# Kernel optimization log

Measured on AMD Instinct MI355X. Metric: run time of the kernel, lower is better.

Reference implementation:

```python
import jax, jax.numpy as jnp
import numpy as np

B, N, D = 1, 4096, 320
HEADS, DIM_HEAD = 8, 40
PHASE, Hm, Wm = 3, 64, 64  # guidance mask spatial dims; Hm*Wm == N


def setup_inputs() -> dict:
    key = jax.random.key(0)
    ks = jax.random.split(key, 7)
    s = 0.02
    x = jax.random.normal(ks[0], (B, N, D), jnp.float32)
    guidance_mask = jax.random.bernoulli(ks[1], 0.25, (B, PHASE, Hm, Wm)).astype(jnp.float32)
    Wq = jax.random.normal(ks[2], (D, HEADS * DIM_HEAD), jnp.float32) * s
    Wk = jax.random.normal(ks[3], (D, HEADS * DIM_HEAD), jnp.float32) * s
    Wv = jax.random.normal(ks[4], (D, HEADS * DIM_HEAD), jnp.float32) * s
    Wo = jax.random.normal(ks[5], (HEADS * DIM_HEAD, D), jnp.float32) * s
    bo = jnp.zeros((D,), jnp.float32)
    return {"x": x, "guidance_mask": guidance_mask, "Wq": Wq, "Wk": Wk,
            "Wv": Wv, "Wo": Wo, "bo": bo}


def reference(x, guidance_mask, Wq, Wk, Wv, Wo, bo):
    b, n, _ = x.shape
    h, dh = HEADS, DIM_HEAD
    scale = dh ** (-0.5)

    def split_heads(t):
        # b n (h d) -> (b h) n d
        return t.reshape(b, n, h, dh).transpose(0, 2, 1, 3).reshape(b * h, n, dh)

    q = split_heads(x @ Wq)
    k = split_heads(x @ Wk)
    v = split_heads(x @ Wv)

    sim = jnp.einsum('bid,bjd->bij', q, k) * scale  # (b*h, n, n)

    _, p, Hh, Ww = guidance_mask.shape
    HW = Hh * Ww  # == n
    g = guidance_mask.reshape(b, p, HW)
    # sum over phases of outer products, clamped at 1 (binary block mask)
    mask_sim = jnp.minimum(jnp.einsum('bpi,bpj->bij', g, g), 1.0)  # (b, HW, HW)
    mask_sim = jnp.repeat(mask_sim, h, axis=0)  # (b*h, HW, HW), heads within each b

    neg = -jnp.finfo(sim.dtype).max
    # original: sim[:, :, :HW][mask_sim == 0] = -max ; here n == HW so full matrix
    sim = jnp.where(mask_sim == 0, neg, sim)

    attn = jax.nn.softmax(sim, axis=-1)
    out = jnp.einsum('bij,bjd->bid', attn, v)  # (b*h, n, dh)
    out = out.reshape(b, h, n, dh).transpose(0, 2, 1, 3).reshape(b, n, h * dh)
    return out @ Wo + bo
```

## Files before the change

kernel.cpp:

```cpp
#include <hip/hip_runtime.h>
#include <hip/hip_bf16.h>
#include <stdint.h>

#define NT 4096
#define DM 320
#define NH 8
#define DH 40
#define KS 4
#define QSCALE 0.22811013f
#define PSTR 68
#define KFJB 640

typedef float f32x4 __attribute__((ext_vector_type(4)));
typedef __bf16 bf16x8 __attribute__((ext_vector_type(8)));

__device__ __forceinline__ unsigned short f2b(float f) {
  unsigned u = __builtin_bit_cast(unsigned, f);
  u += 0x7FFFu + ((u >> 16) & 1u);
  return (unsigned short)(u >> 16);
}

__device__ __forceinline__ bf16x8 ld_bf8(const unsigned short* p) {
  uint4 v = *(const uint4*)p;
  return __builtin_bit_cast(bf16x8, v);
}

__device__ __forceinline__ f32x4 mfma16(bf16x8 a, bf16x8 b, f32x4 c) {
  return __builtin_amdgcn_mfma_f32_16x16x32_bf16(a, b, c, 0, 0, 0);
}

__device__ __forceinline__ float fexp2(float x) {
#if __has_builtin(__builtin_amdgcn_exp2f)
  return __builtin_amdgcn_exp2f(x);
#else
  float r; asm("v_exp_f32 %0, %1" : "=v"(r) : "v"(x)); return r;
#endif
}

__device__ __forceinline__ uint2 pack4(float a, float b, float c, float d) {
  uint2 pk;
  pk.x = (unsigned)f2b(a) | ((unsigned)f2b(b) << 16);
  pk.y = (unsigned)f2b(c) | ((unsigned)f2b(d) << 16);
  return pk;
}

__device__ __forceinline__ size_t fmi(int tile, int nk, int k, int o) {
  return ((size_t)tile * nk + (k >> 5)) * 512 + (size_t)((k >> 3) & 3) * 128 +
         (size_t)(o & 15) * 8 + (k & 7);
}

__global__ __launch_bounds__(256) void prep_kernel(
    const float* __restrict__ x, const float* __restrict__ g,
    const float* __restrict__ Wq, const float* __restrict__ Wk,
    const float* __restrict__ Wv, const float* __restrict__ Wo,
    unsigned short* __restrict__ xbf, unsigned char* __restrict__ sgp,
    unsigned short* __restrict__ Wtf, int* __restrict__ perm,
    int* __restrict__ invp, int* __restrict__ nqp) {
  const int b = blockIdx.x, t = threadIdx.x;
  if (b == 100) {
    __shared__ int cnt[256];
    unsigned char mys[16];
    int c1 = 0;
#pragma unroll
    for (int i = 0; i < 16; ++i) {
      int tok = t * 16 + i;
      unsigned s = 0;
      if (g[tok] != 0.f)          s |= 1u;
      if (g[NT + tok] != 0.f)     s |= 2u;
      if (g[2 * NT + tok] != 0.f) s |= 4u;
      mys[i] = (unsigned char)s;
      c1 += (s != 0u);
    }
    cnt[t] = c1;
    __syncthreads();
    for (int off = 1; off < 256; off <<= 1) {
      int v = (t >= off) ? cnt[t - off] : 0;
      __syncthreads();
      cnt[t] += v;
      __syncthreads();
    }
    const int nq = cnt[255];
    int p1 = cnt[t] - c1;
    int p0 = nq + (t * 16 - p1);
#pragma unroll
    for (int i = 0; i < 16; ++i) {
      int tok = t * 16 + i;
      if (mys[i] != 0) { perm[p1] = tok; invp[tok] = p1; sgp[p1] = mys[i]; p1++; }
      else             { perm[p0] = tok; invp[tok] = p0; sgp[p0] = 0;      p0++; }
    }
    if (t == 0) nqp[0] = nq;
    return;
  }
  if (b > 100) {
    int base = (b - 101) * 2560;
#pragma unroll
    for (int j = 0; j < 10; ++j) {
      int i = (base + j * 256 + t) * 4;
      int m = i / DM, k = i % DM;
      float4 v = *(const float4*)(x + i);
      ushort4 u;
      u.x = f2b(v.x); u.y = f2b(v.y); u.z = f2b(v.z); u.w = f2b(v.w);
      *(ushort4*)(xbf + fmi(m >> 4, 10, k, m)) = u;
    }
    return;
  }
  __shared__ __align__(16) unsigned short lt[64 * 72];
  int kx = b % 5, cy = b / 5;
  int cm = cy % 5;
  const float* src;
  int rowbase;
  if (cy < 5)       { src = Wq; rowbase = cm * 64; }
  else if (cy < 10) { src = Wk; rowbase = 320 + cm * 64; }
  else if (cy < 15) { src = Wv; rowbase = 640 + cm * 64; }
  else              { src = Wo; rowbase = 960 + cm * 64; }
  const int c0 = cm * 64;
  const int k0 = kx * 64;
#pragma unroll
  for (int i = 0; i < 4; ++i) {
    int kr = (t >> 4) + i * 16, cc = (t & 15) * 4;
    float4 w4 = *(const float4*)&src[(size_t)(k0 + kr) * DM + c0 + cc];
    lt[(cc + 0) * 72 + kr] = f2b(w4.x);
    lt[(cc + 1) * 72 + kr] = f2b(w4.y);
    lt[(cc + 2) * 72 + kr] = f2b(w4.z);
    lt[(cc + 3) * 72 + kr] = f2b(w4.w);
  }
  __syncthreads();
#pragma unroll
  for (int i = 0; i < 2; ++i) {
    int idx = t + i * 256, cl = idx >> 3, ch = idx & 7;
    int c = rowbase + cl, k = k0 + ch * 8;
    *(uint4*)&Wtf[fmi(c >> 4, 10, k, c)] = *(const uint4*)&lt[cl * 72 + ch * 8];
  }
}

__global__ __launch_bounds__(256, 4) void qkv_gemm(
    const unsigned short* __restrict__ xbf, const unsigned short* __restrict__ Wtf,
    const int* __restrict__ invp,
    unsigned short* __restrict__ Qb, unsigned short* __restrict__ Kf,
    unsigned short* __restrict__ Vf) {
  const int t = threadIdx.x;
  const int w = t >> 6, lane = t & 63, quad = lane >> 4, ln = lane & 15;
  const int m0 = blockIdx.x * 64;
  const int cy = blockIdx.y;
  const int a = cy / 5;
  const int cc0 = (cy % 5) * 64;
  const int mt = (m0 >> 4) + w;
  const int ct0 = a * 20 + (cc0 >> 4);

  f32x4 acc[4] = {{0,0,0,0},{0,0,0,0},{0,0,0,0},{0,0,0,0}};
  for (int kc = 0; kc < 10; ++kc) {
    bf16x8 xf = ld_bf8(xbf + ((size_t)(mt * 10 + kc)) * 512 + lane * 8);
#pragma unroll
    for (int nt = 0; nt < 4; ++nt) {
      bf16x8 wf = ld_bf8(Wtf + ((size_t)((ct0 + nt) * 10 + kc)) * 512 + lane * 8);
      if (a < 2) acc[nt] = mfma16(wf, xf, acc[nt]);
      else       acc[nt] = mfma16(xf, wf, acc[nt]);
    }
  }
  if (a == 0) {
    const int bp = invp[m0 + w * 16 + ln];
#pragma unroll
    for (int nt = 0; nt < 4; ++nt) {
      int c = cc0 + nt * 16 + quad * 4;
      int h = c / DH, d = c % DH;
      uint2 pk = pack4(acc[nt][0] * QSCALE, acc[nt][1] * QSCALE,
                       acc[nt][2] * QSCALE, acc[nt][3] * QSCALE);
      *(uint2*)&Qb[((size_t)h * NT + bp) * 64 + d] = pk;
    }
  } else if (a == 1) {
    const int bp = invp[m0 + w * 16 + ln];
#pragma unroll
    for (int nt = 0; nt < 4; ++nt) {
      int c = cc0 + nt * 16 + quad * 4;
      int h = c / DH, d = c % DH;
      uint2 pk = pack4(acc[nt][0], acc[nt][1], acc[nt][2], acc[nt][3]);
      size_t base = ((size_t)h * 256 + (bp >> 4)) * KFJB;
      size_t idx = (d < 32)
          ? base + (size_t)(d >> 3) * 128 + (size_t)(bp & 15) * 8 + (d & 7)
          : base + 512 + (size_t)(bp & 15) * 8 + (d - 32);
      *(uint2*)&Kf[idx] = pk;
    }
  } else {
    const int mb = m0 + w * 16 + quad * 4;
    int bpr[4];
#pragma unroll
    for (int r = 0; r < 4; ++r) bpr[r] = invp[mb + r];
#pragma unroll
    for (int nt = 0; nt < 4; ++nt) {
      int c = cc0 + nt * 16 + ln;
      int h = c / DH, d = c % DH;
#pragma unroll
      for (int r = 0; r < 4; ++r) {
        int bp = bpr[r];
        size_t idx = ((((((size_t)(h * 64 + (bp >> 6)) * 3 + (d >> 4)) * 2 +
                         ((bp >> 5) & 1)) * 4 + ((bp >> 3) & 3)) * 16 + (d & 15))) * 8 +
                     (bp & 7);
        Vf[idx] = f2b(acc[nt][r]);
      }
    }
  }
}

__global__ __launch_bounds__(256, 4) void attn_kernel(
    const unsigned short* __restrict__ Qb, const unsigned short* __restrict__ Kf,
    const unsigned short* __restrict__ Vf, const unsigned char* __restrict__ sgp,
    const int* __restrict__ perm, const int* __restrict__ nqp,
    unsigned short* __restrict__ Opf, float* __restrict__ Lpart,
    unsigned short* __restrict__ Ubf) {
  __shared__ __align__(16) unsigned short pt[4][32 * PSTR];
  __shared__ float vs[4][48];
  const int t = threadIdx.x;
  const int w = t >> 6, lane = t & 63, quad = lane >> 4, ln = lane & 15;
  const int h = blockIdx.y, sp = blockIdx.z;
  const int nq = nqp[0];
  const int nkt = (nq + 63) >> 6;
  const int nq_pad = (nq + 127) & ~127;

  const unsigned short* Vfh = Vf + (size_t)h * 196608;
  const uint4 z4 = {0, 0, 0, 0};
  const uint4 ones4 = {0x3F803F80u, 0x3F803F80u, 0x3F803F80u, 0x3F803F80u};
  const bf16x8 onesb = __builtin_bit_cast(bf16x8, ones4);

  if (blockIdx.x == 32) {
    if (sp != 0) return;
    f32x4 o[3] = {{0,0,0,0},{0,0,0,0},{0,0,0,0}};
    for (int jt = w; jt < 64; jt += 4) {
#pragma unroll
      for (int ot = 0; ot < 3; ++ot) {
        uint4 v0 = *(const uint4*)(Vfh + ((size_t)((jt * 3 + ot) * 2 + 0)) * 512 +
                                   lane * 8);
        uint4 v1 = *(const uint4*)(Vfh + ((size_t)((jt * 3 + ot) * 2 + 1)) * 512 +
                                   lane * 8);
        o[ot] = mfma16(__builtin_bit_cast(bf16x8, v0), onesb, o[ot]);
        o[ot] = mfma16(__builtin_bit_cast(bf16x8, v1), onesb, o[ot]);
      }
    }
    if (ln == 0) {
#pragma unroll
      for (int ot = 0; ot < 3; ++ot)
#pragma unroll
        for (int r = 0; r < 4; ++r) vs[w][ot * 16 + quad * 4 + r] = o[ot][r];
    }
    __syncthreads();
    if (t < DH) {
      float s = vs[0][t] + vs[1][t] + vs[2][t] + vs[3][t];
      Ubf[h * DH + t] = f2b(s * (1.0f / (float)NT));
    }
    return;
  }

  const int qt = (blockIdx.x + 8 * sp) & 31;
  if (qt * 128 >= nq_pad) return;
  const int qrow = qt * 128 + w * 32;

  const unsigned short* Kfh = Kf + (size_t)h * 256 * KFJB;
  unsigned short* ptw = pt[w];
  const bool vone = (ln == 8);

  bf16x8 qa[2][2];
  unsigned sqx4[2];
  int morig[2];
  f32x4 o[3][2] = {{{0,0,0,0},{0,0,0,0}},{{0,0,0,0},{0,0,0,0}},{{0,0,0,0},{0,0,0,0}}};

#pragma unroll
  for (int tq = 0; tq < 2; ++tq) {
    int bp = qrow + tq * 16 + ln;
    morig[tq] = perm[bp];
    const unsigned short* Qp = Qb + ((size_t)h * NT + bp) * 64;
    qa[tq][0] = ld_bf8(Qp + quad * 8);
    uint4 q1 = z4;
    if (quad == 0) q1 = *(const uint4*)(Qp + 32);
    qa[tq][1] = __builtin_bit_cast(bf16x8, q1);
    sqx4[tq] = (unsigned)sgp[bp] * 0x01010101u;
  }

  for (int jt = sp; jt < nkt; jt += KS) {
    uint4 kfr0[4], kfr1[4];
#pragma unroll
    for (int nt = 0; nt < 4; ++nt) {
      const unsigned short* kb = Kfh + (size_t)(jt * 4 + nt) * KFJB;
      kfr0[nt] = *(const uint4*)(kb + lane * 8);
      kfr1[nt] = z4;
      if (lane < 16) kfr1[nt] = *(const uint4*)(kb + 512 + lane * 8);
    }
#pragma unroll
    for (int nt = 0; nt < 4; ++nt) {
      bf16x8 ka0 = __builtin_bit_cast(bf16x8, kfr0[nt]);
      bf16x8 ka1 = __builtin_bit_cast(bf16x8, kfr1[nt]);
      unsigned spj = *(const unsigned*)(sgp + jt * 64 + nt * 16 + quad * 4);
#pragma unroll
      for (int tq = 0; tq < 2; ++tq) {
        f32x4 acc = {0.f, 0.f, 0.f, 0.f};
        acc = mfma16(ka0, qa[tq][0], acc);
        acc = mfma16(ka1, qa[tq][1], acc);
        unsigned m4 = spj & sqx4[tq];
        unsigned u[4];
#pragma unroll
        for (int r = 0; r < 4; ++r) {
          unsigned mb = (m4 >> (8 * r)) & 255u;
          float am = mb ? acc[r] : -3.0e38f;
          u[r] = __builtin_bit_cast(unsigned, fexp2(am));
        }
        uint2 pk;
        pk.x = (u[0] >> 16) | (u[1] & 0xffff0000u);
        pk.y = (u[2] >> 16) | (u[3] & 0xffff0000u);
        *(uint2*)&ptw[(tq * 16 + ln) * PSTR + nt * 16 + quad * 4] = pk;
      }
    }
    uint4 vfr[6];
#pragma unroll
    for (int ot = 0; ot < 3; ++ot)
#pragma unroll
      for (int c = 0; c < 2; ++c)
        vfr[ot * 2 + c] =
            *(const uint4*)(Vfh + ((size_t)((jt * 3 + ot) * 2 + c)) * 512 + lane * 8);
    if (vone) { vfr[4] = ones4; vfr[5] = ones4; }

    bf16x8 pb[2][2];
    asm volatile("s_waitcnt lgkmcnt(0)" ::: "memory");
#pragma unroll
    for (int tq = 0; tq < 2; ++tq) {
      pb[tq][0] = ld_bf8(&ptw[(tq * 16 + ln) * PSTR + quad * 8]);
      pb[tq][1] = ld_bf8(&ptw[(tq * 16 + ln) * PSTR + 32 + quad * 8]);
    }
#pragma unroll
    for (int ot = 0; ot < 3; ++ot) {
      bf16x8 va0 = __builtin_bit_cast(bf16x8, vfr[ot * 2]);
      bf16x8 va1 = __builtin_bit_cast(bf16x8, vfr[ot * 2 + 1]);
#pragma unroll
      for (int tq = 0; tq < 2; ++tq) {
        o[ot][tq] = mfma16(va0, pb[tq][0], o[ot][tq]);
        o[ot][tq] = mfma16(va1, pb[tq][1], o[ot][tq]);
      }
    }
  }

#pragma unroll
  for (int tq = 0; tq < 2; ++tq) {
    int m = morig[tq];
#pragma unroll
    for (int ot = 0; ot < 3; ++ot) {
      int d0 = ot * 16 + quad * 4;
      if (d0 < DH) {
        int c = h * DH + d0;
        uint2 pk = pack4(o[ot][tq][0], o[ot][tq][1], o[ot][tq][2], o[ot][tq][3]);
        *(uint2*)&Opf[fmi(sp * 256 + (m >> 4), 10, c, m)] = pk;
      }
    }
    if (quad == 2)
      Lpart[sp * NT + m] = o[2][tq][0];
  }
}

__global__ __launch_bounds__(256, 4) void out_gemm(
    const unsigned short* __restrict__ Opf, const float* __restrict__ Lpart,
    const unsigned short* __restrict__ Wtf, const float* __restrict__ bo,
    const int* __restrict__ invp, const int* __restrict__ nqp,
    const unsigned short* __restrict__ Ubf, float* __restrict__ out) {
  const int t = threadIdx.x;
  const int w = t >> 6, lane = t & 63, quad = lane >> 4, ln = lane & 15;
  const int m0 = blockIdx.x * 64;
  const int cc0 = blockIdx.y * 64;
  const int mt = (m0 >> 4) + w;
  const int m = m0 + w * 16 + ln;
  const int ct0 = 60 + (cc0 >> 4);
  const bool uni = invp[m] >= nqp[0];
  float ls = 0.f;
#pragma unroll
  for (int sp = 0; sp < KS; ++sp) ls += Lpart[sp * NT + m];
  const float inv = 1.f / ls;

  f32x4 acc[4] = {{0,0,0,0},{0,0,0,0},{0,0,0,0},{0,0,0,0}};
  for (int kc = 0; kc < 10; ++kc) {
    uint4 uv = *(const uint4*)(Ubf + kc * 32 + quad * 8);
    float s8[8] = {0, 0, 0, 0, 0, 0, 0, 0};
#pragma unroll
    for (int sp = 0; sp < KS; ++sp) {
      uint4 v = *(const uint4*)(Opf + ((size_t)((sp * 256 + mt) * 10 + kc)) * 512 +
                                lane * 8);
      unsigned vv[4] = {v.x, v.y, v.z, v.w};
#pragma unroll
      for (int j = 0; j < 4; ++j) {
        s8[2 * j]     += __builtin_bit_cast(float, vv[j] << 16);
        s8[2 * j + 1] += __builtin_bit_cast(float, vv[j] & 0xffff0000u);
      }
    }
    uint4 av;
    av.x = (unsigned)f2b(s8[0] * inv) | ((unsigned)f2b(s8[1] * inv) << 16);
    av.y = (unsigned)f2b(s8[2] * inv) | ((unsigned)f2b(s8[3] * inv) << 16);
    av.z = (unsigned)f2b(s8[4] * inv) | ((unsigned)f2b(s8[5] * inv) << 16);
    av.w = (unsigned)f2b(s8[6] * inv) | ((unsigned)f2b(s8[7] * inv) << 16);
    if (uni) av = uv;
    bf16x8 af = __builtin_bit_cast(bf16x8, av);
#pragma unroll
    for (int nt = 0; nt < 4; ++nt) {
      bf16x8 wf = ld_bf8(Wtf + ((size_t)((ct0 + nt) * 10 + kc)) * 512 + lane * 8);
      acc[nt] = mfma16(wf, af, acc[nt]);
    }
  }
#pragma unroll
  for (int nt = 0; nt < 4; ++nt) {
    int c = cc0 + nt * 16 + quad * 4;
    float4 bv = *(const float4*)(bo + c);
    float4 ov;
    ov.x = acc[nt][0] + bv.x;
    ov.y = acc[nt][1] + bv.y;
    ov.z = acc[nt][2] + bv.z;
    ov.w = acc[nt][3] + bv.w;
    *(float4*)(out + (size_t)m * DM + c) = ov;
  }
}

extern "C" void kernel_launch(void* const* d_in, const int* in_sizes, int n_in,
                              void* d_out, int out_size, void* d_ws, size_t ws_size,
                              hipStream_t stream) {
  const float* x  = (const float*)d_in[0];
  const float* g  = (const float*)d_in[1];
  const float* Wq = (const float*)d_in[2];
  const float* Wk = (const float*)d_in[3];
  const float* Wv = (const float*)d_in[4];
  const float* Wo = (const float*)d_in[5];
  const float* bo = (const float*)d_in[6];
  float* out = (float*)d_out;

  char* ws = (char*)d_ws;
  const size_t SGP_OFF  = 0;
  const size_t NQ_OFF   = 4096;
  const size_t PERM_OFF = 8192;
  const size_t INV_OFF  = 24576;
  const size_t XBF_OFF  = 40960;
  const size_t WTF_OFF = XBF_OFF + (size_t)NT * DM * 2;
  const size_t QB_OFF  = WTF_OFF + (size_t)1280 * DM * 2;
  const size_t KF_OFF  = QB_OFF + (size_t)NH * NT * 64 * 2;
  const size_t VF_OFF  = KF_OFF + (size_t)NH * 256 * KFJB * 2;
  const size_t OPF_OFF = VF_OFF + (size_t)NH * 196608 * 2;
  const size_t LP_OFF  = OPF_OFF + (size_t)KS * 256 * 10 * 512 * 2;
  const size_t UBF_OFF = LP_OFF + (size_t)KS * NT * 4;
  unsigned char* sgp   = (unsigned char*)(ws + SGP_OFF);
  int* nqp             = (int*)(ws + NQ_OFF);
  int* perm            = (int*)(ws + PERM_OFF);
  int* invp            = (int*)(ws + INV_OFF);
  unsigned short* xbf  = (unsigned short*)(ws + XBF_OFF);
  unsigned short* Wtf  = (unsigned short*)(ws + WTF_OFF);
  unsigned short* Qb   = (unsigned short*)(ws + QB_OFF);
  unsigned short* Kf   = (unsigned short*)(ws + KF_OFF);
  unsigned short* Vf   = (unsigned short*)(ws + VF_OFF);
  unsigned short* Opf  = (unsigned short*)(ws + OPF_OFF);
  float* Lpart         = (float*)(ws + LP_OFF);
  unsigned short* Ubf  = (unsigned short*)(ws + UBF_OFF);

  prep_kernel<<<229, 256, 0, stream>>>(x, g, Wq, Wk, Wv, Wo, xbf, sgp, Wtf,
                                       perm, invp, nqp);
  qkv_gemm<<<dim3(64, 15), 256, 0, stream>>>(xbf, Wtf, invp, Qb, Kf, Vf);
  attn_kernel<<<dim3(33, NH, KS), 256, 0, stream>>>(Qb, Kf, Vf, sgp, perm, nqp,
                                                    Opf, Lpart, Ubf);
  out_gemm<<<dim3(64, 5), 256, 0, stream>>>(Opf, Lpart, Wtf, bo, invp, nqp,
                                            Ubf, out);
}
```

Before: 135.8 us.

## Move V retiling and split-K combine into separate coalesced kernels

The QKV GEMM now writes V in the same fragment layout as K, using uint2 stores instead of scattered 2-byte stores. A new retile kernel uses identity-matrix MFMAs to transpose V into the layout the attention kernel expects. The split-K partial combine and row un-permutation move out of the output GEMM into a dedicated combine kernel that writes a bf16 fragment buffer. Attention now writes outputs in permuted order. This trades extra launches and an extra round trip through global memory for coalesced writes and less redundant combine work across the output GEMM's column blocks.

```diff
diff --git a/kernel.cpp b/kernel.cpp
--- a/kernel.cpp
+++ b/kernel.cpp
@@ -42,6 +42,15 @@
   pk.x = (unsigned)f2b(a) | ((unsigned)f2b(b) << 16);
   pk.y = (unsigned)f2b(c) | ((unsigned)f2b(d) << 16);
   return pk;
+}
+
+__device__ __forceinline__ uint4 idfrag(int idx) {
+  uint4 r;
+  r.x = (idx == 0 ? 0x3F80u : 0u) | (idx == 1 ? 0x3F800000u : 0u);
+  r.y = (idx == 2 ? 0x3F80u : 0u) | (idx == 3 ? 0x3F800000u : 0u);
+  r.z = (idx == 4 ? 0x3F80u : 0u) | (idx == 5 ? 0x3F800000u : 0u);
+  r.w = (idx == 6 ? 0x3F80u : 0u) | (idx == 7 ? 0x3F800000u : 0u);
+  return r;
 }
 
 __device__ __forceinline__ size_t fmi(int tile, int nk, int k, int o) {
@@ -137,7 +146,7 @@
     const unsigned short* __restrict__ xbf, const unsigned short* __restrict__ Wtf,
     const int* __restrict__ invp,
     unsigned short* __restrict__ Qb, unsigned short* __restrict__ Kf,
-    unsigned short* __restrict__ Vf) {
+    unsigned short* __restrict__ Vk) {
   const int t = threadIdx.x;
   const int w = t >> 6, lane = t & 63, quad = lane >> 4, ln = lane & 15;
   const int m0 = blockIdx.x * 64;
@@ -153,12 +162,11 @@
 #pragma unroll
     for (int nt = 0; nt < 4; ++nt) {
       bf16x8 wf = ld_bf8(Wtf + ((size_t)((ct0 + nt) * 10 + kc)) * 512 + lane * 8);
-      if (a < 2) acc[nt] = mfma16(wf, xf, acc[nt]);
-      else       acc[nt] = mfma16(xf, wf, acc[nt]);
-    }
-  }
+      acc[nt] = mfma16(wf, xf, acc[nt]);
+    }
+  }
+  const int bp = invp[m0 + w * 16 + ln];
   if (a == 0) {
-    const int bp = invp[m0 + w * 16 + ln];
 #pragma unroll
     for (int nt = 0; nt < 4; ++nt) {
       int c = cc0 + nt * 16 + quad * 4;
@@ -167,8 +175,8 @@
                        acc[nt][2] * QSCALE, acc[nt][3] * QSCALE);
       *(uint2*)&Qb[((size_t)h * NT + bp) * 64 + d] = pk;
     }
-  } else if (a == 1) {
-    const int bp = invp[m0 + w * 16 + ln];
+  } else {
+    unsigned short* dst = (a == 1) ? Kf : Vk;
 #pragma unroll
     for (int nt = 0; nt < 4; ++nt) {
       int c = cc0 + nt * 16 + quad * 4;
@@ -178,25 +186,40 @@
       size_t idx = (d < 32)
           ? base + (size_t)(d >> 3) * 128 + (size_t)(bp & 15) * 8 + (d & 7)
           : base + 512 + (size_t)(bp & 15) * 8 + (d - 32);
-      *(uint2*)&Kf[idx] = pk;
-    }
-  } else {
-    const int mb = m0 + w * 16 + quad * 4;
-    int bpr[4];
-#pragma unroll
-    for (int r = 0; r < 4; ++r) bpr[r] = invp[mb + r];
-#pragma unroll
-    for (int nt = 0; nt < 4; ++nt) {
-      int c = cc0 + nt * 16 + ln;
-      int h = c / DH, d = c % DH;
-#pragma unroll
-      for (int r = 0; r < 4; ++r) {
-        int bp = bpr[r];
-        size_t idx = ((((((size_t)(h * 64 + (bp >> 6)) * 3 + (d >> 4)) * 2 +
-                         ((bp >> 5) & 1)) * 4 + ((bp >> 3) & 3)) * 16 + (d & 15))) * 8 +
-                     (bp & 7);
-        Vf[idx] = f2b(acc[nt][r]);
-      }
+      *(uint2*)&dst[idx] = pk;
+    }
+  }
+}
+
+__global__ __launch_bounds__(256) void retile_kernel(
+    const unsigned short* __restrict__ Vk, unsigned short* __restrict__ Vf) {
+  const int t = threadIdx.x;
+  const int w = t >> 6, lane = t & 63, ln = lane & 15, jg = lane >> 4;
+  const bf16x8 b1f = __builtin_bit_cast(bf16x8, idfrag(ln - jg * 8));
+  const bf16x8 b2f = __builtin_bit_cast(bf16x8, idfrag(ln + 16 - jg * 8));
+  const uint4 z4 = {0, 0, 0, 0};
+#pragma unroll
+  for (int i = 0; i < 4; ++i) {
+    const int task = (blockIdx.x * 4 + w) * 4 + i;
+    const int h = task >> 8, jb = task & 255;
+    const unsigned short* kb = Vk + ((size_t)h * 256 + jb) * KFJB;
+    uint4 f0 = *(const uint4*)(kb + lane * 8);
+    uint4 f1 = z4;
+    if (lane < 16) f1 = *(const uint4*)(kb + 512 + lane * 8);
+    f32x4 d1 = {0,0,0,0}, d2 = {0,0,0,0}, d3 = {0,0,0,0};
+    d1 = mfma16(__builtin_bit_cast(bf16x8, f0), b1f, d1);
+    d2 = mfma16(__builtin_bit_cast(bf16x8, f0), b2f, d2);
+    d3 = mfma16(__builtin_bit_cast(bf16x8, f1), b1f, d3);
+    const int bp = jb * 16 + jg * 4;
+#pragma unroll
+    for (int ot = 0; ot < 3; ++ot) {
+      int dd = ot * 16 + ln;
+      if (ot == 2 && ln >= 8) continue;
+      f32x4 dv = (ot == 0) ? d1 : (ot == 1) ? d2 : d3;
+      size_t idx = ((((((size_t)(h * 64 + (bp >> 6)) * 3 + (dd >> 4)) * 2 +
+                       ((bp >> 5) & 1)) * 4 + ((bp >> 3) & 3)) * 16 + (dd & 15))) * 8 +
+                   (bp & 7);
+      *(uint2*)&Vf[idx] = pack4(dv[0], dv[1], dv[2], dv[3]);
     }
   }
 }
@@ -204,7 +227,7 @@
 __global__ __launch_bounds__(256, 4) void attn_kernel(
     const unsigned short* __restrict__ Qb, const unsigned short* __restrict__ Kf,
     const unsigned short* __restrict__ Vf, const unsigned char* __restrict__ sgp,
-    const int* __restrict__ perm, const int* __restrict__ nqp,
+    const int* __restrict__ nqp,
     unsigned short* __restrict__ Opf, float* __restrict__ Lpart,
     unsigned short* __restrict__ Ubf) {
   __shared__ __align__(16) unsigned short pt[4][32 * PSTR];
@@ -259,13 +282,11 @@
 
   bf16x8 qa[2][2];
   unsigned sqx4[2];
-  int morig[2];
   f32x4 o[3][2] = {{{0,0,0,0},{0,0,0,0}},{{0,0,0,0},{0,0,0,0}},{{0,0,0,0},{0,0,0,0}}};
 
 #pragma unroll
   for (int tq = 0; tq < 2; ++tq) {
     int bp = qrow + tq * 16 + ln;
-    morig[tq] = perm[bp];
     const unsigned short* Qp = Qb + ((size_t)h * NT + bp) * 64;
     qa[tq][0] = ld_bf8(Qp + quad * 8);
     uint4 q1 = z4;
@@ -337,26 +358,64 @@
 
 #pragma unroll
   for (int tq = 0; tq < 2; ++tq) {
-    int m = morig[tq];
+    int bp = qrow + tq * 16 + ln;
 #pragma unroll
     for (int ot = 0; ot < 3; ++ot) {
       int d0 = ot * 16 + quad * 4;
       if (d0 < DH) {
         int c = h * DH + d0;
         uint2 pk = pack4(o[ot][tq][0], o[ot][tq][1], o[ot][tq][2], o[ot][tq][3]);
-        *(uint2*)&Opf[fmi(sp * 256 + (m >> 4), 10, c, m)] = pk;
+        *(uint2*)&Opf[fmi(sp * 256 + (bp >> 4), 10, c, bp)] = pk;
       }
     }
     if (quad == 2)
-      Lpart[sp * NT + m] = o[2][tq][0];
-  }
+      Lpart[sp * NT + bp] = o[2][tq][0];
+  }
+}
+
+__global__ __launch_bounds__(256, 4) void combine_kernel(
+    const unsigned short* __restrict__ Opf, const float* __restrict__ Lpart,
+    const int* __restrict__ perm, const int* __restrict__ nqp,
+    unsigned short* __restrict__ Abf) {
+  const int t = threadIdx.x;
+  const int w = t >> 6, lane = t & 63;
+  const int task = blockIdx.x * 4 + w;
+  const int tile = task / 10, kc = task % 10;
+  const int nq_pad = (nqp[0] + 127) & ~127;
+  if (tile * 16 >= nq_pad) return;
+  const int row = tile * 16 + (lane & 15);
+
+  float L = 0.f;
+#pragma unroll
+  for (int sp = 0; sp < KS; ++sp) L += Lpart[sp * NT + row];
+  const float inv = 1.f / L;
+
+  float s8[8] = {0, 0, 0, 0, 0, 0, 0, 0};
+#pragma unroll
+  for (int sp = 0; sp < KS; ++sp) {
+    uint4 v = *(const uint4*)(Opf + ((size_t)((sp * 256 + tile) * 10 + kc)) * 512 +
+                              lane * 8);
+    unsigned vv[4] = {v.x, v.y, v.z, v.w};
+#pragma unroll
+    for (int j = 0; j < 4; ++j) {
+      s8[2 * j]     += __builtin_bit_cast(float, vv[j] << 16);
+      s8[2 * j + 1] += __builtin_bit_cast(float, vv[j] & 0xffff0000u);
+    }
+  }
+  uint4 av;
+  av.x = (unsigned)f2b(s8[0] * inv) | ((unsigned)f2b(s8[1] * inv) << 16);
+  av.y = (unsigned)f2b(s8[2] * inv) | ((unsigned)f2b(s8[3] * inv) << 16);
+  av.z = (unsigned)f2b(s8[4] * inv) | ((unsigned)f2b(s8[5] * inv) << 16);
+  av.w = (unsigned)f2b(s8[6] * inv) | ((unsigned)f2b(s8[7] * inv) << 16);
+  const int m = perm[row];
+  *(uint4*)&Abf[fmi(m >> 4, 10, kc * 32 + (lane >> 4) * 8, m)] = av;
 }
 
 __global__ __launch_bounds__(256, 4) void out_gemm(
-    const unsigned short* __restrict__ Opf, const float* __restrict__ Lpart,
-    const unsigned short* __restrict__ Wtf, const float* __restrict__ bo,
-    const int* __restrict__ invp, const int* __restrict__ nqp,
-    const unsigned short* __restrict__ Ubf, float* __restrict__ out) {
+    const unsigned short* __restrict__ Abf, const unsigned short* __restrict__ Wtf,
+    const float* __restrict__ bo, const int* __restrict__ invp,
+    const int* __restrict__ nqp, const unsigned short* __restrict__ Ubf,
+    float* __restrict__ out) {
   const int t = threadIdx.x;
   const int w = t >> 6, lane = t & 63, quad = lane >> 4, ln = lane & 15;
   const int m0 = blockIdx.x * 64;
@@ -365,31 +424,11 @@
   const int m = m0 + w * 16 + ln;
   const int ct0 = 60 + (cc0 >> 4);
   const bool uni = invp[m] >= nqp[0];
-  float ls = 0.f;
-#pragma unroll
-  for (int sp = 0; sp < KS; ++sp) ls += Lpart[sp * NT + m];
-  const float inv = 1.f / ls;
 
   f32x4 acc[4] = {{0,0,0,0},{0,0,0,0},{0,0,0,0},{0,0,0,0}};
   for (int kc = 0; kc < 10; ++kc) {
     uint4 uv = *(const uint4*)(Ubf + kc * 32 + quad * 8);
-    float s8[8] = {0, 0, 0, 0, 0, 0, 0, 0};
-#pragma unroll
-    for (int sp = 0; sp < KS; ++sp) {
-      uint4 v = *(const uint4*)(Opf + ((size_t)((sp * 256 + mt) * 10 + kc)) * 512 +
-                                lane * 8);
-      unsigned vv[4] = {v.x, v.y, v.z, v.w};
-#pragma unroll
-      for (int j = 0; j < 4; ++j) {
-        s8[2 * j]     += __builtin_bit_cast(float, vv[j] << 16);
-        s8[2 * j + 1] += __builtin_bit_cast(float, vv[j] & 0xffff0000u);
-      }
-    }
-    uint4 av;
-    av.x = (unsigned)f2b(s8[0] * inv) | ((unsigned)f2b(s8[1] * inv) << 16);
-    av.y = (unsigned)f2b(s8[2] * inv) | ((unsigned)f2b(s8[3] * inv) << 16);
-    av.z = (unsigned)f2b(s8[4] * inv) | ((unsigned)f2b(s8[5] * inv) << 16);
-    av.w = (unsigned)f2b(s8[6] * inv) | ((unsigned)f2b(s8[7] * inv) << 16);
+    uint4 av = *(const uint4*)(Abf + ((size_t)(mt * 10 + kc)) * 512 + lane * 8);
     if (uni) av = uv;
     bf16x8 af = __builtin_bit_cast(bf16x8, av);
 #pragma unroll
@@ -432,10 +471,12 @@
   const size_t WTF_OFF = XBF_OFF + (size_t)NT * DM * 2;
   const size_t QB_OFF  = WTF_OFF + (size_t)1280 * DM * 2;
   const size_t KF_OFF  = QB_OFF + (size_t)NH * NT * 64 * 2;
-  const size_t VF_OFF  = KF_OFF + (size_t)NH * 256 * KFJB * 2;
+  const size_t VK_OFF  = KF_OFF + (size_t)NH * 256 * KFJB * 2;
+  const size_t VF_OFF  = VK_OFF + (size_t)NH * 256 * KFJB * 2;
   const size_t OPF_OFF = VF_OFF + (size_t)NH * 196608 * 2;
   const size_t LP_OFF  = OPF_OFF + (size_t)KS * 256 * 10 * 512 * 2;
   const size_t UBF_OFF = LP_OFF + (size_t)KS * NT * 4;
+  const size_t ABF_OFF = UBF_OFF + 4096;
   unsigned char* sgp   = (unsigned char*)(ws + SGP_OFF);
   int* nqp             = (int*)(ws + NQ_OFF);
   int* perm            = (int*)(ws + PERM_OFF);
@@ -444,16 +485,19 @@
   unsigned short* Wtf  = (unsigned short*)(ws + WTF_OFF);
   unsigned short* Qb   = (unsigned short*)(ws + QB_OFF);
   unsigned short* Kf   = (unsigned short*)(ws + KF_OFF);
+  unsigned short* Vk   = (unsigned short*)(ws + VK_OFF);
   unsigned short* Vf   = (unsigned short*)(ws + VF_OFF);
   unsigned short* Opf  = (unsigned short*)(ws + OPF_OFF);
   float* Lpart         = (float*)(ws + LP_OFF);
   unsigned short* Ubf  = (unsigned short*)(ws + UBF_OFF);
+  unsigned short* Abf  = (unsigned short*)(ws + ABF_OFF);
 
   prep_kernel<<<229, 256, 0, stream>>>(x, g, Wq, Wk, Wv, Wo, xbf, sgp, Wtf,
                                        perm, invp, nqp);
-  qkv_gemm<<<dim3(64, 15), 256, 0, stream>>>(xbf, Wtf, invp, Qb, Kf, Vf);
-  attn_kernel<<<dim3(33, NH, KS), 256, 0, stream>>>(Qb, Kf, Vf, sgp, perm, nqp,
+  qkv_gemm<<<dim3(64, 15), 256, 0, stream>>>(xbf, Wtf, invp, Qb, Kf, Vk);
+  retile_kernel<<<128, 256, 0, stream>>>(Vk, Vf);
+  attn_kernel<<<dim3(33, NH, KS), 256, 0, stream>>>(Qb, Kf, Vf, sgp, nqp,
                                                     Opf, Lpart, Ubf);
-  out_gemm<<<dim3(64, 5), 256, 0, stream>>>(Opf, Lpart, Wtf, bo, invp, nqp,
-                                            Ubf, out);
-}
+  combine_kernel<<<640, 256, 0, stream>>>(Opf, Lpart, perm, nqp, Abf);
+  out_gemm<<<dim3(64, 5), 256, 0, stream>>>(Abf, Wtf, bo, invp, nqp, Ubf, out);
+}
```

Measured after the change: 130.9 us. -3.6%, faster.
